# Performance work log

Measured on AMD Instinct MI355X. Metric: run time of the kernel, lower is better.

The kernel has to match this reference:

```python
import jax, jax.numpy as jnp
import numpy as np
from jax import lax

H, W = 3072, 4096
BLACK = 0.0625            # black level (normalized)
KNEE_X = np.array([0.0, 0.25, 1.0], np.float32)   # decompanding curve
KNEE_Y = np.array([0.0, 0.50, 1.0], np.float32)
DEN_R, DEN_EPS = 2, 100.0         # BayerDenoise defaults
AWB_MAX_GAIN = 4.0
LTM_A, LTM_B, LTM_R, LTM_EPS = 0.7, 0.0, 8, 1e-3
GAMMA = 2.2


def _box_sum_1d(x, r, axis):
    """Sliding-window sum of width 2r+1 along `axis`, edge-truncated."""
    n = x.shape[axis]
    c = jnp.cumsum(x, axis=axis)
    hi = jnp.clip(jnp.arange(n) + r, 0, n - 1)
    lo = jnp.arange(n) - r - 1
    upper = jnp.take(c, hi, axis=axis)
    lower = jnp.take(c, jnp.clip(lo, 0, n - 1), axis=axis)
    shp = [1] * x.ndim
    shp[axis] = n
    lower = lower * (lo >= 0).astype(x.dtype).reshape(shp)
    return upper - lower


def box_mean(x, r):
    """2D box mean over last two axes, normalized by valid window counts."""
    s = _box_sum_1d(_box_sum_1d(x, r, -2), r, -1)
    cnt = _box_sum_1d(_box_sum_1d(jnp.ones_like(x), r, -2), r, -1)
    return s / cnt


def guided_self(I, r, eps):
    """Self-guided (edge-preserving) filter."""
    m = box_mean(I, r)
    var = box_mean(I * I, r) - m * m
    a = var / (var + eps)
    b = m * (1.0 - a)
    return box_mean(a, r) * I + box_mean(b, r)


def conv3x3(img, k):
    return lax.conv_general_dilated(img[None, None], k[None, None], (1, 1), 'SAME')[0, 0]


def isp_pipeline(x, ccm):
    # --- DecompandBlackLevel: piecewise-linear decompand + black level ---
    x = jnp.interp(x, jnp.asarray(KNEE_X), jnp.asarray(KNEE_Y))
    x = jnp.clip((x - BLACK) / (1.0 - BLACK), 0.0, 1.0)

    # --- BayerDenoise: guided filter on each RGGB plane ---
    p = jnp.stack([x[0::2, 0::2], x[0::2, 1::2], x[1::2, 0::2], x[1::2, 1::2]])  # [4,H/2,W/2]
    p = guided_self(p, DEN_R, DEN_EPS)

    # --- AWB: gray-world gains from plane means (lum mask [0,1] = all pixels) ---
    r_m, g_m, b_m = p[0].mean(), 0.5 * (p[1].mean() + p[2].mean()), p[3].mean()
    gr = jnp.minimum(g_m / (r_m + 1e-8), AWB_MAX_GAIN)
    gb = jnp.minimum(g_m / (b_m + 1e-8), AWB_MAX_GAIN)
    x = (jnp.zeros_like(x)
         .at[0::2, 0::2].set(jnp.clip(p[0] * gr, 0.0, 1.0))
         .at[0::2, 1::2].set(jnp.clip(p[1], 0.0, 1.0))
         .at[1::2, 0::2].set(jnp.clip(p[2], 0.0, 1.0))
         .at[1::2, 1::2].set(jnp.clip(p[3] * gb, 0.0, 1.0)))

    # --- Demosaic: bilinear on RGGB mosaic ---
    ii = (jnp.arange(H) % 2)[:, None]
    jj = (jnp.arange(W) % 2)[None, :]
    mR = ((ii == 0) & (jj == 0)).astype(x.dtype)
    mG = (ii != jj).astype(x.dtype)
    mB = ((ii == 1) & (jj == 1)).astype(x.dtype)
    k_g = jnp.array([[0, 1, 0], [1, 4, 1], [0, 1, 0]], jnp.float32) / 4.0
    k_rb = jnp.array([[1, 2, 1], [2, 4, 2], [1, 2, 1]], jnp.float32) / 4.0
    rgb = jnp.stack([conv3x3(x * mR, k_rb), conv3x3(x * mG, k_g), conv3x3(x * mB, k_rb)])  # [3,H,W]

    # --- CCM ---
    rgb = jnp.clip(jnp.einsum('ij,jhw->ihw', ccm, rgb), 0.0, 1.0)

    wl = jnp.array([0.299, 0.587, 0.114], jnp.float32)
    Y = jnp.einsum('c,chw->hw', wl, rgb)
    Ys = Y.reshape(H // 2, 2, W // 2, 2).mean(axis=(1, 3))
    base = jax.image.resize(guided_self(Ys, LTM_R, LTM_EPS), (H, W), 'bilinear')
    Ynew = LTM_A * base + LTM_B + (Y - base)       # detail_gain=1, threshold=0
    rgb = jnp.clip(rgb * (Ynew / (Y + 1e-6)), 0.0, 1.0)

    # --- Gamma ---
    rgb = jnp.clip(rgb, 1e-6, 1.0) ** (1.0 / GAMMA)
    # hist_norm / post_denoise / saturation / sharpening are identity at defaults

    # --- RGBtoYUV -> NV12 (full range BT.601) ---
    R, G, B = rgb[0], rgb[1], rgb[2]
    Yf = 0.299 * R + 0.587 * G + 0.114 * B
    U = -0.168736 * R - 0.331264 * G + 0.5 * B + 0.5
    V = 0.5 * R - 0.418688 * G - 0.081312 * B + 0.5
    Us = U.reshape(H // 2, 2, W // 2, 2).mean(axis=(1, 3))
    Vs = V.reshape(H // 2, 2, W // 2, 2).mean(axis=(1, 3))
    uv = jnp.stack([Us, Vs], axis=-1).reshape(H // 2, W)  # interleaved UVUV...
    out = jnp.concatenate([Yf.reshape(-1), uv.reshape(-1)]) * 255.0
    return jnp.clip(out, 0.0, 255.0)   # float NV12 codes (pre-quantization)


def setup_inputs() -> dict:
    key = jax.random.key(0)
    k1, k2 = jax.random.split(key)
    x = jax.random.uniform(k1, (H, W), dtype=jnp.float32)
    ccm = jnp.eye(3, dtype=jnp.float32) + 0.1 * jax.random.normal(k2, (3, 3), dtype=jnp.float32)
    return {"x": x, "ccm": ccm}


def reference(x, ccm):
    return isp_pipeline(x, ccm)
```

## Files before the change

### kernel.cpp

```cpp
#include <hip/hip_runtime.h>
#include <math.h>

#define IMG_H 3072
#define IMG_W 4096
#define Hh 1536
#define Wh 2048
#define S (Hh*Wh)

#define TID 32
#define TVL 16
#define HBLK 192

#if __has_builtin(__builtin_amdgcn_rcpf)
#define RCP(x) __builtin_amdgcn_rcpf(x)
#else
#define RCP(x) (1.0f/(x))
#endif

__device__ __forceinline__ float clamp01(float v){ return fminf(fmaxf(v, 0.0f), 1.0f); }

__device__ __forceinline__ float decompand_black(float v){
  float y = (v <= 0.25f) ? (2.0f*v) : fmaf(v - 0.25f, 0.5f/0.75f, 0.5f);
  y = clamp01(y);
  return clamp01((y - 0.0625f) * (1.0f/0.9375f));
}

__device__ __forceinline__ float gamma22(float x){
  return __builtin_amdgcn_exp2f(0.45454545454545453f * __builtin_amdgcn_logf(x));
}

__global__ __launch_bounds__(256) void k_split(const float* __restrict__ x, float* __restrict__ P,
                                               float* __restrict__ sums){
  int idx = blockIdx.x*256 + threadIdx.x;
  int i = idx >> 10, jq = (idx & 1023)*2;
  const float* r0 = x + (size_t)(2*i)*IMG_W + 2*jq;
  float4 a = *(const float4*)r0;
  float4 b = *(const float4*)(r0 + IMG_W);
  size_t o = (size_t)i*Wh + jq;
  *(float2*)(P + o)            = make_float2(decompand_black(a.x), decompand_black(a.z));
  *(float2*)(P + S + o)        = make_float2(decompand_black(a.y), decompand_black(a.w));
  *(float2*)(P + 2*(size_t)S + o) = make_float2(decompand_black(b.x), decompand_black(b.z));
  *(float2*)(P + 3*(size_t)S + o) = make_float2(decompand_black(b.y), decompand_black(b.w));
  if (blockIdx.x == 0 && threadIdx.x < 4) sums[threadIdx.x] = 0.f;
}

template<int TI, bool FAST>
__device__ __forceinline__ void denoise_col2(const float* __restrict__ in, float* __restrict__ D,
                                             int c0, int i0, float& local){
  const float inv25 = 1.0f/25.0f;
  float cw_a[6], amask[6], cw_o0 = 25.f, cw_o1 = 25.f;
  if (!FAST){
    #pragma unroll
    for (int k=0;k<6;++k){
      int pc = c0 + k - 2;
      bool ok = ((unsigned)pc < (unsigned)Wh);
      amask[k] = ok ? 1.f : 0.f;
      cw_a[k]  = ok ? (float)(min(pc+2, Wh-1) - max(pc-2, 0) + 1) : 1.f;
    }
    cw_o0 = (float)(min(c0+2, Wh-1)   - max(c0-2, 0) + 1);
    cw_o1 = (float)(min(c0+3, Wh-1)   - max(c0-1, 0) + 1);
  }

  float rh1[6][5]={{0}}, rh2[6][5]={{0}};
  float vs1[6]={0}, vs2[6]={0};
  float rha0[5]={0}, rhb0[5]={0}, rha1[5]={0}, rhb1[5]={0};
  float cI0[5]={0}, cI1[5]={0};
  float wa0=0.f, wb0=0.f, wa1=0.f, wb1=0.f;

  const float* rp = in + (size_t)(i0-4)*Wh + c0;
  float* wp = D + (size_t)i0*Wh + c0;

  #pragma unroll 5
  for (int rr=0; rr<TI+8; ++rr){
    int r = i0 - 4 + rr;
    float v[10];
    if (FAST){
      float2 p0 = *(const float2*)(rp-4);
      float2 p1 = *(const float2*)(rp-2);
      float2 p2 = *(const float2*)(rp);
      float2 p3 = *(const float2*)(rp+2);
      float2 p4 = *(const float2*)(rp+4);
      v[0]=p0.x; v[1]=p0.y; v[2]=p1.x; v[3]=p1.y; v[4]=p2.x;
      v[5]=p2.y; v[6]=p3.x; v[7]=p3.y; v[8]=p4.x; v[9]=p4.y;
    } else {
      if ((unsigned)r < (unsigned)Hh){
        #pragma unroll
        for (int d=0; d<10; ++d){
          int c = c0 + d - 4;
          v[d] = ((unsigned)c < (unsigned)Wh) ? rp[d-4] : 0.f;
        }
      } else {
        #pragma unroll
        for (int d=0; d<10; ++d) v[d]=0.f;
      }
    }
    rp += Wh;
    float sq[10];
    #pragma unroll
    for (int d=0; d<10; ++d) sq[d]=v[d]*v[d];
    float h1[6], h2[6];
    h1[0]=v[0]+v[1]+v[2]+v[3]+v[4];
    h2[0]=sq[0]+sq[1]+sq[2]+sq[3]+sq[4];
    #pragma unroll
    for (int k=1;k<6;++k){
      h1[k]=h1[k-1]-v[k-1]+v[k+4];
      h2[k]=h2[k-1]-sq[k-1]+sq[k+4];
    }
    #pragma unroll
    for (int k=0;k<6;++k){
      vs1[k]+=h1[k]-rh1[k][0];
      vs2[k]+=h2[k]-rh2[k][0];
      #pragma unroll
      for (int t=0;t<4;++t){ rh1[k][t]=rh1[k][t+1]; rh2[k][t]=rh2[k][t+1]; }
      rh1[k][4]=h1[k]; rh2[k][4]=h2[k];
    }
    #pragma unroll
    for (int t=0;t<4;++t){ cI0[t]=cI0[t+1]; cI1[t]=cI1[t+1]; }
    cI0[4]=v[4]; cI1[4]=v[5];

    if (rr >= 4){
      int q = r-2;
      float a6[6], b6[6];
      if (FAST){
        #pragma unroll
        for (int k=0;k<6;++k){
          float m   = vs1[k]*inv25;
          float var = fmaf(-m, m, vs2[k]*inv25);
          float a   = var*RCP(var + 100.0f);
          a6[k] = a; b6[k] = fmaf(-m, a, m);
        }
      } else {
        float rmask = ((unsigned)q < (unsigned)Hh) ? 1.f : 0.f;
        float rh = (float)(min(q+2, Hh-1) - max(q-2, 0) + 1);
        #pragma unroll
        for (int k=0;k<6;++k){
          float inv = RCP(rh*cw_a[k]);
          float m   = vs1[k]*inv;
          float var = fmaf(-m, m, vs2[k]*inv);
          float a   = var*RCP(var + 100.0f);
          float b   = fmaf(-m, a, m);
          a6[k] = a*amask[k]*rmask; b6[k] = b*amask[k]*rmask;
        }
      }
      float ha0 = a6[0]+a6[1]+a6[2]+a6[3]+a6[4];
      float hb0 = b6[0]+b6[1]+b6[2]+b6[3]+b6[4];
      float ha1 = ha0 - a6[0] + a6[5];
      float hb1 = hb0 - b6[0] + b6[5];
      wa0 += ha0 - rha0[0]; wb0 += hb0 - rhb0[0];
      wa1 += ha1 - rha1[0]; wb1 += hb1 - rhb1[0];
      #pragma unroll
      for (int t=0;t<4;++t){
        rha0[t]=rha0[t+1]; rhb0[t]=rhb0[t+1];
        rha1[t]=rha1[t+1]; rhb1[t]=rhb1[t+1];
      }
      rha0[4]=ha0; rhb0[4]=hb0; rha1[4]=ha1; rhb1[4]=hb1;

      if (rr >= 8){
        int ro = r-4;
        float invo0, invo1;
        if (FAST){ invo0 = inv25; invo1 = inv25; }
        else {
          float rho = (float)(min(ro+2, Hh-1) - max(ro-2, 0) + 1);
          invo0 = RCP(rho*cw_o0); invo1 = RCP(rho*cw_o1);
        }
        float d0 = fmaf(wa0*invo0, cI0[0], wb0*invo0);
        float d1 = fmaf(wa1*invo1, cI1[0], wb1*invo1);
        *(float2*)wp = make_float2(d0, d1); wp += Wh;
        local += d0 + d1;
      }
    }
  }
}

template<int TI>
__global__ __launch_bounds__(256) void k_denoise(const float* __restrict__ P4,
                                                 float* __restrict__ D4,
                                                 float* __restrict__ sums){
  const int c0 = (blockIdx.x*256 + threadIdx.x)*2;
  const int i0 = blockIdx.y*TI;
  const int pl = blockIdx.z;
  const float* __restrict__ in = P4 + (size_t)pl*S;
  float* __restrict__ D = D4 + (size_t)pl*S;
  float local = 0.f;

  const int cmin = (blockIdx.x*256 + (threadIdx.x & ~63))*2;
  const bool rows_ok = (i0 >= 4) && (i0 + TI + 4 <= Hh);
  const bool fast = rows_ok && (cmin >= 4) && (cmin + 131 < Wh);
  if (fast) denoise_col2<TI, true >(in, D, c0, i0, local);
  else      denoise_col2<TI, false>(in, D, c0, i0, local);

  __shared__ float red[256];
  red[threadIdx.x]=local;
  __syncthreads();
  #pragma unroll
  for (int off=128; off>0; off>>=1){
    if (threadIdx.x<off) red[threadIdx.x]+=red[threadIdx.x+off];
    __syncthreads();
  }
  if (threadIdx.x==0) atomicAdd(sums+pl, red[0]);
}

template<bool SQUARE>
__global__ __launch_bounds__(256) void k_ltm_h(const float* __restrict__ X1,
                                               const float* __restrict__ X2,
                                               float* __restrict__ O1,
                                               float* __restrict__ O2){
  const int lane = threadIdx.x & 63;
  const int wave = threadIdx.x >> 6;
  const int row  = blockIdx.y;
  const int ob   = blockIdx.x*HBLK + wave*48;
  const int c    = ob - 8 + lane;
  const size_t rb = (size_t)row*Wh;

  float v1 = 0.f, v2 = 0.f;
  if ((unsigned)c < (unsigned)Wh){
    v1 = X1[rb + c];
    v2 = SQUARE ? v1*v1 : X2[rb + c];
  }
  #pragma unroll
  for (int d=1; d<64; d<<=1){
    float t1 = __shfl_up(v1, d, 64);
    float t2 = __shfl_up(v2, d, 64);
    if (lane >= d){ v1 += t1; v2 += t2; }
  }
  float hi1 = __shfl_down(v1, 16, 64);
  float hi2 = __shfl_down(v2, 16, 64);
  float lo1 = __shfl_up(v1, 1, 64);
  float lo2 = __shfl_up(v2, 1, 64);
  if (lane == 0){ lo1 = 0.f; lo2 = 0.f; }
  int oc = ob + lane;
  if (lane < 48 && oc < Wh){
    O1[rb + oc] = hi1 - lo1;
    O2[rb + oc] = hi2 - lo2;
  }
}

template<int TV>
__global__ __launch_bounds__(256) void k_ltm_v_ab(const float* __restrict__ H1,
                                                  const float* __restrict__ H2,
                                                  float* __restrict__ A,
                                                  float* __restrict__ B){
  const int j  = blockIdx.x*256 + threadIdx.x;
  const int i0 = blockIdx.y*TV;
  const float cwf = (float)(min(j+8, Wh-1) - max(j-8, 0) + 1);
  float ws1 = 0.f, ws2 = 0.f;
  #pragma unroll
  for (int k=-8; k<=8; ++k){
    int r = i0 + k;
    if ((unsigned)r < (unsigned)Hh){
      ws1 += H1[(size_t)r*Wh + j];
      ws2 += H2[(size_t)r*Wh + j];
    }
  }
  #pragma unroll
  for (int t=0; t<TV; ++t){
    int i = i0 + t;
    float rhf = (float)(min(i+8, Hh-1) - max(i-8, 0) + 1);
    float inv = 1.0f/(rhf*cwf);
    float m   = ws1*inv;
    float var = fmaf(-m, m, ws2*inv);
    float a   = var/(var + 1e-3f);
    A[(size_t)i*Wh + j] = a;
    B[(size_t)i*Wh + j] = m*(1.0f - a);
    if (t < TV-1){
      int rn = i+9, ro = i-8;
      float n1=0.f, n2=0.f, o1=0.f, o2=0.f;
      if (rn < Hh){ n1 = H1[(size_t)rn*Wh + j]; n2 = H2[(size_t)rn*Wh + j]; }
      if (ro >= 0){ o1 = H1[(size_t)ro*Wh + j]; o2 = H2[(size_t)ro*Wh + j]; }
      ws1 += n1 - o1; ws2 += n2 - o2;
    }
  }
}

template<int TV>
__global__ __launch_bounds__(256) void k_ltm_v_fin(const float* __restrict__ Ha,
                                                   const float* __restrict__ Hb,
                                                   const float* __restrict__ Ysrc,
                                                   float* __restrict__ bs){
  const int j  = blockIdx.x*256 + threadIdx.x;
  const int i0 = blockIdx.y*TV;
  const float cwf = (float)(min(j+8, Wh-1) - max(j-8, 0) + 1);
  float wa = 0.f, wb = 0.f;
  #pragma unroll
  for (int k=-8; k<=8; ++k){
    int r = i0 + k;
    if ((unsigned)r < (unsigned)Hh){
      wa += Ha[(size_t)r*Wh + j];
      wb += Hb[(size_t)r*Wh + j];
    }
  }
  #pragma unroll
  for (int t=0; t<TV; ++t){
    int i = i0 + t;
    float rhf = (float)(min(i+8, Hh-1) - max(i-8, 0) + 1);
    float inv = 1.0f/(rhf*cwf);
    bs[(size_t)i*Wh + j] = fmaf(wa*inv, Ysrc[(size_t)i*Wh + j], wb*inv);
    if (t < TV-1){
      int rn = i+9, ro = i-8;
      float na=0.f, nb=0.f, oa=0.f, ob_=0.f;
      if (rn < Hh){ na = Ha[(size_t)rn*Wh + j]; nb = Hb[(size_t)rn*Wh + j]; }
      if (ro >= 0){ oa = Ha[(size_t)ro*Wh + j]; ob_ = Hb[(size_t)ro*Wh + j]; }
      wa += na - oa; wb += nb - ob_;
    }
  }
}

__device__ __forceinline__ void awb_gains(const float* __restrict__ sums, float& gr, float& gb){
  const float invS = 1.0f/(float)S;
  float rm = sums[0]*invS, g1 = sums[1]*invS, g2 = sums[2]*invS, bm = sums[3]*invS;
  float gm = 0.5f*(g1+g2);
  gr = fminf(gm/(rm + 1e-8f), 4.0f);
  gb = fminf(gm/(bm + 1e-8f), 4.0f);
}

__device__ __forceinline__ void load_mosaic2(const float* __restrict__ D, float gr, float gb,
                                             int i, int j, float m[4][6]){
  const float* __restrict__ P0 = D;
  const float* __restrict__ P1 = D + (size_t)S;
  const float* __restrict__ P2 = D + (size_t)2*S;
  const float* __restrict__ P3 = D + (size_t)3*S;
  const bool up = (i > 0), dn = (i < Hh-1), lf = (j > 0), rt = (j+2 < Wh);
  const size_t rc = (size_t)i*Wh + j;
  const size_t ru = rc - Wh, rd = rc + Wh;
  const float2 z = make_float2(0.f, 0.f);
  {
    float2 t3 = up ? *(const float2*)(P3+ru) : z;
    float2 t2 = up ? *(const float2*)(P2+ru) : z;
    m[0][0] = (up&&lf) ? clamp01(P3[ru-1]*gb) : 0.f;
    m[0][1] = clamp01(t2.x);
    m[0][2] = clamp01(t3.x*gb);
    m[0][3] = clamp01(t2.y);
    m[0][4] = clamp01(t3.y*gb);
    m[0][5] = (up&&rt) ? clamp01(P2[ru+2]) : 0.f;
  }
  {
    float2 t1 = *(const float2*)(P1+rc);
    float2 t0 = *(const float2*)(P0+rc);
    m[1][0] = lf ? clamp01(P1[rc-1]) : 0.f;
    m[1][1] = clamp01(t0.x*gr);
    m[1][2] = clamp01(t1.x);
    m[1][3] = clamp01(t0.y*gr);
    m[1][4] = clamp01(t1.y);
    m[1][5] = rt ? clamp01(P0[rc+2]*gr) : 0.f;
  }
  {
    float2 s3 = *(const float2*)(P3+rc);
    float2 s2 = *(const float2*)(P2+rc);
    m[2][0] = lf ? clamp01(P3[rc-1]*gb) : 0.f;
    m[2][1] = clamp01(s2.x);
    m[2][2] = clamp01(s3.x*gb);
    m[2][3] = clamp01(s2.y);
    m[2][4] = clamp01(s3.y*gb);
    m[2][5] = rt ? clamp01(P2[rc+2]) : 0.f;
  }
  {
    float2 u1 = dn ? *(const float2*)(P1+rd) : z;
    float2 u0 = dn ? *(const float2*)(P0+rd) : z;
    m[3][0] = (dn&&lf) ? clamp01(P1[rd-1]) : 0.f;
    m[3][1] = clamp01(u0.x*gr);
    m[3][2] = clamp01(u1.x);
    m[3][3] = clamp01(u0.y*gr);
    m[3][4] = clamp01(u1.y);
    m[3][5] = (dn&&rt) ? clamp01(P0[rd+2]*gr) : 0.f;
  }
}

template<int O>
__device__ __forceinline__ void demosaic_ccm_s(const float m[4][6], const float* __restrict__ C,
                                               float R[2][2], float G[2][2], float Bv[2][2]){
  #define MM(a,b) m[a][(b)+2*O]
  float r[2][2], g[2][2], b[2][2];
  r[0][0] = MM(1,1);
  g[0][0] = 0.25f*(MM(0,1)+MM(2,1)+MM(1,0)+MM(1,2));
  b[0][0] = 0.25f*(MM(0,0)+MM(0,2)+MM(2,0)+MM(2,2));
  r[0][1] = 0.5f*(MM(1,1)+MM(1,3));
  g[0][1] = MM(1,2);
  b[0][1] = 0.5f*(MM(0,2)+MM(2,2));
  r[1][0] = 0.5f*(MM(1,1)+MM(3,1));
  g[1][0] = MM(2,1);
  b[1][0] = 0.5f*(MM(2,0)+MM(2,2));
  r[1][1] = 0.25f*(MM(1,1)+MM(1,3)+MM(3,1)+MM(3,3));
  g[1][1] = 0.25f*(MM(1,2)+MM(3,2)+MM(2,1)+MM(2,3));
  b[1][1] = MM(2,2);
  #undef MM
  #pragma unroll
  for (int a=0; a<2; ++a){
    #pragma unroll
    for (int c=0; c<2; ++c){
      R[a][c]  = clamp01(fmaf(C[2], b[a][c], fmaf(C[1], g[a][c], C[0]*r[a][c])));
      G[a][c]  = clamp01(fmaf(C[5], b[a][c], fmaf(C[4], g[a][c], C[3]*r[a][c])));
      Bv[a][c] = clamp01(fmaf(C[8], b[a][c], fmaf(C[7], g[a][c], C[6]*r[a][c])));
    }
  }
}

__global__ __launch_bounds__(256) void k_ys(const float* __restrict__ D, const float* __restrict__ sums,
                                            const float* __restrict__ C, float* __restrict__ Ys){
  int idx = blockIdx.x*256 + threadIdx.x;
  int i = idx >> 10, j = (idx & 1023)*2;
  float gr, gb; awb_gains(sums, gr, gb);
  float m[4][6]; load_mosaic2(D, gr, gb, i, j, m);
  float y0 = 0.f, y1 = 0.f;
  {
    float R[2][2], G[2][2], Bv[2][2];
    demosaic_ccm_s<0>(m, C, R, G, Bv);
    #pragma unroll
    for (int a=0; a<2; ++a)
      #pragma unroll
      for (int c=0; c<2; ++c)
        y0 += 0.299f*R[a][c] + 0.587f*G[a][c] + 0.114f*Bv[a][c];
  }
  {
    float R[2][2], G[2][2], Bv[2][2];
    demosaic_ccm_s<1>(m, C, R, G, Bv);
    #pragma unroll
    for (int a=0; a<2; ++a)
      #pragma unroll
      for (int c=0; c<2; ++c)
        y1 += 0.299f*R[a][c] + 0.587f*G[a][c] + 0.114f*Bv[a][c];
  }
  *(float2*)(Ys + (size_t)i*Wh + j) = make_float2(0.25f*y0, 0.25f*y1);
}

__global__ __launch_bounds__(256) void k_final(const float* __restrict__ D, const float* __restrict__ sums,
                                               const float* __restrict__ C,
                                               const float* __restrict__ bs, float* __restrict__ out){
  int idx = blockIdx.x*256 + threadIdx.x;
  int i = idx >> 10, j = (idx & 1023)*2;
  float gr, gb; awb_gains(sums, gr, gb);
  float m[4][6]; load_mosaic2(D, gr, gb, i, j, m);

  float bsv[3][4];
  #pragma unroll
  for (int a=0; a<3; ++a){
    int r = min(max(i-1+a, 0), Hh-1);
    const float* br = bs + ((size_t)r<<11);
    bsv[a][0] = br[max(j-1, 0)];
    float2 t = *(const float2*)(br + j);
    bsv[a][1] = t.x; bsv[a][2] = t.y;
    bsv[a][3] = br[min(j+2, Wh-1)];
  }

  float Yrow0[4], Yrow1[4], UV[4];
  #pragma unroll
  for (int o=0; o<2; ++o){
    float R[2][2], G[2][2], Bv[2][2];
    if (o==0) demosaic_ccm_s<0>(m, C, R, G, Bv);
    else      demosaic_ccm_s<1>(m, C, R, G, Bv);
    float base[2][2];
    base[0][0] = 0.0625f*bsv[0][0+o] + 0.1875f*bsv[0][1+o] + 0.1875f*bsv[1][0+o] + 0.5625f*bsv[1][1+o];
    base[0][1] = 0.1875f*bsv[0][1+o] + 0.0625f*bsv[0][2+o] + 0.5625f*bsv[1][1+o] + 0.1875f*bsv[1][2+o];
    base[1][0] = 0.1875f*bsv[1][0+o] + 0.5625f*bsv[1][1+o] + 0.0625f*bsv[2][0+o] + 0.1875f*bsv[2][1+o];
    base[1][1] = 0.5625f*bsv[1][1+o] + 0.1875f*bsv[1][2+o] + 0.1875f*bsv[2][1+o] + 0.0625f*bsv[2][2+o];

    float Uacc = 0.f, Vacc = 0.f;
    #pragma unroll
    for (int a=0; a<2; ++a){
      #pragma unroll
      for (int c=0; c<2; ++c){
        float Yl   = 0.299f*R[a][c] + 0.587f*G[a][c] + 0.114f*Bv[a][c];
        float Ynew = fmaf(0.7f, base[a][c], Yl - base[a][c]);
        float sc   = Ynew/(Yl + 1e-6f);
        float Rg = gamma22(fmaxf(clamp01(R[a][c]*sc),  1e-6f));
        float Gg = gamma22(fmaxf(clamp01(G[a][c]*sc),  1e-6f));
        float Bg = gamma22(fmaxf(clamp01(Bv[a][c]*sc), 1e-6f));
        float Yf = 0.299f*Rg + 0.587f*Gg + 0.114f*Bg;
        float Yq = fminf(fmaxf(Yf*255.0f, 0.0f), 255.0f);
        if (a==0) Yrow0[2*o+c] = Yq; else Yrow1[2*o+c] = Yq;
        Uacc += -0.168736f*Rg - 0.331264f*Gg + 0.5f*Bg + 0.5f;
        Vacc +=  0.5f*Rg - 0.418688f*Gg - 0.081312f*Bg + 0.5f;
      }
    }
    UV[2*o]   = fminf(fmaxf(0.25f*Uacc*255.0f, 0.0f), 255.0f);
    UV[2*o+1] = fminf(fmaxf(0.25f*Vacc*255.0f, 0.0f), 255.0f);
  }
  *(float4*)(out + (size_t)(2*i)*IMG_W   + 2*j) = make_float4(Yrow0[0], Yrow0[1], Yrow0[2], Yrow0[3]);
  *(float4*)(out + (size_t)(2*i+1)*IMG_W + 2*j) = make_float4(Yrow1[0], Yrow1[1], Yrow1[2], Yrow1[3]);
  *(float4*)(out + (size_t)IMG_H*IMG_W + (size_t)i*IMG_W + 2*j) = make_float4(UV[0], UV[1], UV[2], UV[3]);
}

extern "C" void kernel_launch(void* const* d_in, const int* in_sizes, int n_in,
                              void* d_out, int out_size, void* d_ws, size_t ws_size,
                              hipStream_t stream){
  const float* x   = (const float*)d_in[0];
  const float* ccm = (const float*)d_in[1];
  float* ws  = (float*)d_ws;
  float* out = (float*)d_out;

  size_t need = ((size_t)10*S + 8)*sizeof(float);
  if (ws_size < need) return;

  float* P   = ws;
  float* D   = ws + (size_t)4*S;
  float* Ys  = ws + (size_t)8*S;
  float* Hs1 = ws;
  float* Hs2 = ws + (size_t)S;
  float* A   = ws + (size_t)2*S;
  float* Bb  = ws + (size_t)3*S;
  float* Ha  = ws;
  float* Hb  = ws + (size_t)S;
  float* bs  = ws + (size_t)2*S;
  float* sums = ws + (size_t)10*S;

  const int nb2 = S/512;
  dim3 gdn(Wh/512, Hh/TID, 4);
  dim3 gh((Wh + HBLK - 1)/HBLK, Hh);
  dim3 gv(Wh/256, Hh/TVL);

  k_split<<<nb2, 256, 0, stream>>>(x, P, sums);
  k_denoise<TID><<<gdn, 256, 0, stream>>>(P, D, sums);
  k_ys<<<nb2, 256, 0, stream>>>(D, sums, ccm, Ys);
  k_ltm_h<true ><<<gh, 256, 0, stream>>>(Ys, Ys, Hs1, Hs2);
  k_ltm_v_ab<TVL><<<gv, 256, 0, stream>>>(Hs1, Hs2, A, Bb);
  k_ltm_h<false><<<gh, 256, 0, stream>>>(A, Bb, Ha, Hb);
  k_ltm_v_fin<TVL><<<gv, 256, 0, stream>>>(Ha, Hb, Ys, bs);
  k_final<<<nb2, 256, 0, stream>>>(D, sums, ccm, bs, out);
}
```

Before: 283.6 us.

## Share guided-filter a/b horizontal sums across lanes via wave shuffles

Each thread in the denoise kernel now computes only its own two columns of the first-stage mean/variance and the a/b coefficients, instead of recomputing six columns of halo redundantly. The neighbouring a/b values for the second horizontal box sum come from adjacent lanes through shfl_up/shfl_down. This cuts the ALU work and global loads per thread. In exchange, each 64-wide wave outputs only 124 columns because the edge lanes act as halo, so some lanes idle on output and the grid grows. Blocks shrink to one wave, and the shared-memory reduction is replaced with a shuffle reduction.

```diff
diff --git a/kernel.cpp b/kernel.cpp
--- a/kernel.cpp
+++ b/kernel.cpp
@@ -10,6 +10,7 @@
 #define TID 32
 #define TVL 16
 #define HBLK 192
+#define DW  124
 
 #if __has_builtin(__builtin_amdgcn_rcpf)
 #define RCP(x) __builtin_amdgcn_rcpf(x)
@@ -45,107 +46,102 @@
 }
 
 template<int TI, bool FAST>
-__device__ __forceinline__ void denoise_col2(const float* __restrict__ in, float* __restrict__ D,
-                                             int c0, int i0, float& local){
+__device__ __forceinline__ void denoise_w2(const float* __restrict__ in, float* __restrict__ D,
+                                           int ca0, int lane, int i0, float& local){
   const float inv25 = 1.0f/25.0f;
-  float cw_a[6], amask[6], cw_o0 = 25.f, cw_o1 = 25.f;
+  float cw0 = 25.f, cw1 = 25.f, am0 = 1.f, am1 = 1.f;
   if (!FAST){
-    #pragma unroll
-    for (int k=0;k<6;++k){
-      int pc = c0 + k - 2;
-      bool ok = ((unsigned)pc < (unsigned)Wh);
-      amask[k] = ok ? 1.f : 0.f;
-      cw_a[k]  = ok ? (float)(min(pc+2, Wh-1) - max(pc-2, 0) + 1) : 1.f;
-    }
-    cw_o0 = (float)(min(c0+2, Wh-1)   - max(c0-2, 0) + 1);
-    cw_o1 = (float)(min(c0+3, Wh-1)   - max(c0-1, 0) + 1);
-  }
-
-  float rh1[6][5]={{0}}, rh2[6][5]={{0}};
-  float vs1[6]={0}, vs2[6]={0};
+    bool ok0 = ((unsigned)ca0     < (unsigned)Wh);
+    bool ok1 = ((unsigned)(ca0+1) < (unsigned)Wh);
+    am0 = ok0 ? 1.f : 0.f;  am1 = ok1 ? 1.f : 0.f;
+    cw0 = ok0 ? (float)(min(ca0+2, Wh-1) - max(ca0-2, 0) + 1) : 1.f;
+    cw1 = ok1 ? (float)(min(ca0+3, Wh-1) - max(ca0-1, 0) + 1) : 1.f;
+  }
+
+  float rh1[2][5]={{0}}, rh2[2][5]={{0}};
+  float vs1[2]={0}, vs2[2]={0};
   float rha0[5]={0}, rhb0[5]={0}, rha1[5]={0}, rhb1[5]={0};
   float cI0[5]={0}, cI1[5]={0};
   float wa0=0.f, wb0=0.f, wa1=0.f, wb1=0.f;
-
-  const float* rp = in + (size_t)(i0-4)*Wh + c0;
-  float* wp = D + (size_t)i0*Wh + c0;
+  const bool outlane = ((unsigned)(lane-1) < 62u);
+
+  const float* rp = in + (size_t)(i0-4)*Wh + ca0;
+  float* wp = D + (size_t)i0*Wh + ca0;
 
   #pragma unroll 5
   for (int rr=0; rr<TI+8; ++rr){
     int r = i0 - 4 + rr;
-    float v[10];
+    float v[6];
     if (FAST){
-      float2 p0 = *(const float2*)(rp-4);
-      float2 p1 = *(const float2*)(rp-2);
-      float2 p2 = *(const float2*)(rp);
-      float2 p3 = *(const float2*)(rp+2);
-      float2 p4 = *(const float2*)(rp+4);
-      v[0]=p0.x; v[1]=p0.y; v[2]=p1.x; v[3]=p1.y; v[4]=p2.x;
-      v[5]=p2.y; v[6]=p3.x; v[7]=p3.y; v[8]=p4.x; v[9]=p4.y;
+      float2 p0 = *(const float2*)(rp-2);
+      float2 p1 = *(const float2*)(rp);
+      float2 p2 = *(const float2*)(rp+2);
+      v[0]=p0.x; v[1]=p0.y; v[2]=p1.x; v[3]=p1.y; v[4]=p2.x; v[5]=p2.y;
     } else {
       if ((unsigned)r < (unsigned)Hh){
         #pragma unroll
-        for (int d=0; d<10; ++d){
-          int c = c0 + d - 4;
-          v[d] = ((unsigned)c < (unsigned)Wh) ? rp[d-4] : 0.f;
+        for (int d=0; d<6; ++d){
+          int c = ca0 + d - 2;
+          v[d] = ((unsigned)c < (unsigned)Wh) ? rp[d-2] : 0.f;
         }
       } else {
         #pragma unroll
-        for (int d=0; d<10; ++d) v[d]=0.f;
+        for (int d=0; d<6; ++d) v[d]=0.f;
       }
     }
     rp += Wh;
-    float sq[10];
+    float sq[6];
     #pragma unroll
-    for (int d=0; d<10; ++d) sq[d]=v[d]*v[d];
-    float h1[6], h2[6];
-    h1[0]=v[0]+v[1]+v[2]+v[3]+v[4];
-    h2[0]=sq[0]+sq[1]+sq[2]+sq[3]+sq[4];
+    for (int d=0; d<6; ++d) sq[d]=v[d]*v[d];
+    float h10 = v[0]+v[1]+v[2]+v[3]+v[4];
+    float h11 = h10 - v[0] + v[5];
+    float h20 = sq[0]+sq[1]+sq[2]+sq[3]+sq[4];
+    float h21 = h20 - sq[0] + sq[5];
+    vs1[0] += h10 - rh1[0][0];  vs1[1] += h11 - rh1[1][0];
+    vs2[0] += h20 - rh2[0][0];  vs2[1] += h21 - rh2[1][0];
     #pragma unroll
-    for (int k=1;k<6;++k){
-      h1[k]=h1[k-1]-v[k-1]+v[k+4];
-      h2[k]=h2[k-1]-sq[k-1]+sq[k+4];
-    }
-    #pragma unroll
-    for (int k=0;k<6;++k){
-      vs1[k]+=h1[k]-rh1[k][0];
-      vs2[k]+=h2[k]-rh2[k][0];
-      #pragma unroll
-      for (int t=0;t<4;++t){ rh1[k][t]=rh1[k][t+1]; rh2[k][t]=rh2[k][t+1]; }
-      rh1[k][4]=h1[k]; rh2[k][4]=h2[k];
-    }
-    #pragma unroll
-    for (int t=0;t<4;++t){ cI0[t]=cI0[t+1]; cI1[t]=cI1[t+1]; }
-    cI0[4]=v[4]; cI1[4]=v[5];
+    for (int t=0;t<4;++t){
+      rh1[0][t]=rh1[0][t+1]; rh1[1][t]=rh1[1][t+1];
+      rh2[0][t]=rh2[0][t+1]; rh2[1][t]=rh2[1][t+1];
+      cI0[t]=cI0[t+1]; cI1[t]=cI1[t+1];
+    }
+    rh1[0][4]=h10; rh1[1][4]=h11; rh2[0][4]=h20; rh2[1][4]=h21;
+    cI0[4]=v[2]; cI1[4]=v[3];
 
     if (rr >= 4){
       int q = r-2;
-      float a6[6], b6[6];
+      float a0,b0,a1,b1;
       if (FAST){
-        #pragma unroll
-        for (int k=0;k<6;++k){
-          float m   = vs1[k]*inv25;
-          float var = fmaf(-m, m, vs2[k]*inv25);
-          float a   = var*RCP(var + 100.0f);
-          a6[k] = a; b6[k] = fmaf(-m, a, m);
-        }
+        float m0   = vs1[0]*inv25;
+        float var0 = fmaf(-m0, m0, vs2[0]*inv25);
+        a0 = var0*RCP(var0 + 100.0f);
+        b0 = fmaf(-m0, a0, m0);
+        float m1   = vs1[1]*inv25;
+        float var1 = fmaf(-m1, m1, vs2[1]*inv25);
+        a1 = var1*RCP(var1 + 100.0f);
+        b1 = fmaf(-m1, a1, m1);
       } else {
         float rmask = ((unsigned)q < (unsigned)Hh) ? 1.f : 0.f;
         float rh = (float)(min(q+2, Hh-1) - max(q-2, 0) + 1);
-        #pragma unroll
-        for (int k=0;k<6;++k){
-          float inv = RCP(rh*cw_a[k]);
-          float m   = vs1[k]*inv;
-          float var = fmaf(-m, m, vs2[k]*inv);
-          float a   = var*RCP(var + 100.0f);
-          float b   = fmaf(-m, a, m);
-          a6[k] = a*amask[k]*rmask; b6[k] = b*amask[k]*rmask;
-        }
+        float inv0 = RCP(rh*cw0);
+        float m0   = vs1[0]*inv0;
+        float var0 = fmaf(-m0, m0, vs2[0]*inv0);
+        float aa0  = var0*RCP(var0 + 100.0f);
+        a0 = aa0*am0*rmask;
+        b0 = fmaf(-m0, aa0, m0)*am0*rmask;
+        float inv1 = RCP(rh*cw1);
+        float m1   = vs1[1]*inv1;
+        float var1 = fmaf(-m1, m1, vs2[1]*inv1);
+        float aa1  = var1*RCP(var1 + 100.0f);
+        a1 = aa1*am1*rmask;
+        b1 = fmaf(-m1, aa1, m1)*am1*rmask;
       }
-      float ha0 = a6[0]+a6[1]+a6[2]+a6[3]+a6[4];
-      float hb0 = b6[0]+b6[1]+b6[2]+b6[3]+b6[4];
-      float ha1 = ha0 - a6[0] + a6[5];
-      float hb1 = hb0 - b6[0] + b6[5];
+      float s_a = a0 + a1, s_b = b0 + b1;
+      float ha0 = __shfl_up(s_a,1,64) + s_a + __shfl_down(a0,1,64);
+      float hb0 = __shfl_up(s_b,1,64) + s_b + __shfl_down(b0,1,64);
+      float ha1 = __shfl_up(a1,1,64)  + s_a + __shfl_down(s_a,1,64);
+      float hb1 = __shfl_up(b1,1,64)  + s_b + __shfl_down(s_b,1,64);
+
       wa0 += ha0 - rha0[0]; wb0 += hb0 - rhb0[0];
       wa1 += ha1 - rha1[0]; wb1 += hb1 - rhb1[0];
       #pragma unroll
@@ -161,43 +157,45 @@
         if (FAST){ invo0 = inv25; invo1 = inv25; }
         else {
           float rho = (float)(min(ro+2, Hh-1) - max(ro-2, 0) + 1);
-          invo0 = RCP(rho*cw_o0); invo1 = RCP(rho*cw_o1);
+          invo0 = RCP(rho*cw0); invo1 = RCP(rho*cw1);
         }
         float d0 = fmaf(wa0*invo0, cI0[0], wb0*invo0);
         float d1 = fmaf(wa1*invo1, cI1[0], wb1*invo1);
-        *(float2*)wp = make_float2(d0, d1); wp += Wh;
-        local += d0 + d1;
+        if (FAST){
+          if (outlane){ *(float2*)wp = make_float2(d0, d1); local += d0 + d1; }
+        } else {
+          if (outlane){
+            if ((unsigned)ca0     < (unsigned)Wh){ wp[0] = d0; local += d0; }
+            if ((unsigned)(ca0+1) < (unsigned)Wh){ wp[1] = d1; local += d1; }
+          }
+        }
+        wp += Wh;
       }
     }
   }
 }
 
 template<int TI>
-__global__ __launch_bounds__(256) void k_denoise(const float* __restrict__ P4,
-                                                 float* __restrict__ D4,
-                                                 float* __restrict__ sums){
-  const int c0 = (blockIdx.x*256 + threadIdx.x)*2;
-  const int i0 = blockIdx.y*TI;
-  const int pl = blockIdx.z;
+__global__ __launch_bounds__(64) void k_denoise(const float* __restrict__ P4,
+                                                float* __restrict__ D4,
+                                                float* __restrict__ sums){
+  const int lane = threadIdx.x;
+  const int ow   = blockIdx.x*DW;
+  const int ca0  = ow - 2 + 2*lane;
+  const int i0   = blockIdx.y*TI;
+  const int pl   = blockIdx.z;
   const float* __restrict__ in = P4 + (size_t)pl*S;
   float* __restrict__ D = D4 + (size_t)pl*S;
   float local = 0.f;
 
-  const int cmin = (blockIdx.x*256 + (threadIdx.x & ~63))*2;
   const bool rows_ok = (i0 >= 4) && (i0 + TI + 4 <= Hh);
-  const bool fast = rows_ok && (cmin >= 4) && (cmin + 131 < Wh);
-  if (fast) denoise_col2<TI, true >(in, D, c0, i0, local);
-  else      denoise_col2<TI, false>(in, D, c0, i0, local);
-
-  __shared__ float red[256];
-  red[threadIdx.x]=local;
-  __syncthreads();
-  #pragma unroll
-  for (int off=128; off>0; off>>=1){
-    if (threadIdx.x<off) red[threadIdx.x]+=red[threadIdx.x+off];
-    __syncthreads();
-  }
-  if (threadIdx.x==0) atomicAdd(sums+pl, red[0]);
+  const bool fast = rows_ok && (ow >= 4) && (ow + 128 <= Wh);
+  if (fast) denoise_w2<TI, true >(in, D, ca0, lane, i0, local);
+  else      denoise_w2<TI, false>(in, D, ca0, lane, i0, local);
+
+  #pragma unroll
+  for (int off=32; off>0; off>>=1) local += __shfl_down(local, off, 64);
+  if (lane==0) atomicAdd(sums+pl, local);
 }
 
 template<bool SQUARE>
@@ -503,12 +501,12 @@
   float* sums = ws + (size_t)10*S;
 
   const int nb2 = S/512;
-  dim3 gdn(Wh/512, Hh/TID, 4);
+  dim3 gdn((Wh + DW - 1)/DW, Hh/TID, 4);
   dim3 gh((Wh + HBLK - 1)/HBLK, Hh);
   dim3 gv(Wh/256, Hh/TVL);
 
   k_split<<<nb2, 256, 0, stream>>>(x, P, sums);
-  k_denoise<TID><<<gdn, 256, 0, stream>>>(P, D, sums);
+  k_denoise<TID><<<gdn, 64, 0, stream>>>(P, D, sums);
   k_ys<<<nb2, 256, 0, stream>>>(D, sums, ccm, Ys);
   k_ltm_h<true ><<<gh, 256, 0, stream>>>(Ys, Ys, Hs1, Hs2);
   k_ltm_v_ab<TVL><<<gv, 256, 0, stream>>>(Hs1, Hs2, A, Bb);
```

After: 304.6 us. +7.4%, slower.
